# Optimization experiments

Hardware: AMD Instinct MI355X
Metric: run time of the kernel (lower is better)

## Reference

```python
import jax, jax.numpy as jnp
import numpy as np

B, S, E = 4, 2048, 1024
N, H = 16, 64  # n_head, per-head hidden


def setup_inputs() -> dict:
    key = jax.random.key(0)
    k1, k2, k3, k4, k5 = jax.random.split(key, 5)
    scale_in = 1.0 / np.sqrt(E)
    scale_h = 1.0 / np.sqrt(N * H)
    return {
        "x": jax.random.normal(k1, (B, S, E), dtype=jnp.float32),
        "W_qkv": jax.random.uniform(k2, (E, 3 * N * H), minval=-scale_in, maxval=scale_in, dtype=jnp.float32),
        "b_qkv": jax.random.uniform(k3, (3 * N * H,), minval=-scale_in, maxval=scale_in, dtype=jnp.float32),
        "W_out": jax.random.uniform(k4, (N * H, E), minval=-scale_h, maxval=scale_h, dtype=jnp.float32),
        "b_out": jax.random.uniform(k5, (E,), minval=-scale_h, maxval=scale_h, dtype=jnp.float32),
    }


def reference(x, W_qkv, b_qkv, W_out, b_out):
    b, s, e = x.shape
    qkv = x @ W_qkv + b_qkv                      # [B,S,3NH]
    q, k, v = jnp.split(qkv, 3, axis=-1)
    q = q.reshape(b, s, N, H).transpose(0, 2, 1, 3)  # [B,N,S,H]
    k = k.reshape(b, s, N, H).transpose(0, 2, 1, 3)
    v = v.reshape(b, s, N, H).transpose(0, 2, 1, 3)
    inv_scale = jnp.asarray(1.0 / np.sqrt(H), dtype=x.dtype)
    attn = jnp.einsum('bnqh,bnkh->bnqk', q, k) * inv_scale  # [B,N,S,S]
    causal = jnp.tril(jnp.ones((s, s), dtype=bool))
    attn = jnp.where(causal[None, None], attn, jnp.asarray(-jnp.inf, dtype=attn.dtype))
    attn = jax.nn.softmax(attn, axis=-1)
    out = jnp.einsum('bnqk,bnkh->bnqh', attn, v)  # [B,N,S,H]
    out = out.transpose(0, 2, 1, 3).reshape(b, s, N * H)
    return out @ W_out + b_out
```

## Files before the change

kernel.cpp:

```cpp
#include <hip/hip_runtime.h>
#include <hip/hip_bf16.h>

typedef __attribute__((ext_vector_type(8))) short s16x8;
typedef __attribute__((ext_vector_type(4))) short s16x4;
typedef __attribute__((ext_vector_type(4))) float f32x4;

#define MFMA16(a, b, c) __builtin_amdgcn_mfma_f32_16x16x32_bf16(a, b, c, 0, 0, 0)

__device__ __forceinline__ short f2bf(float f) {
  unsigned int x = __builtin_bit_cast(unsigned int, f);
  x += 0x7fffu + ((x >> 16) & 1u);
  return (short)(x >> 16);
}

__device__ __forceinline__ int cperm(int k) {
  return ((k & 12) << 1) | ((k >> 4) << 2) | (k & 3);
}

#define LDT 40

__global__ void cvt_f32_bf16(const float* __restrict__ in, short* __restrict__ out, int n) {
  int idx = blockIdx.x * blockDim.x + threadIdx.x;
  int stride = gridDim.x * blockDim.x;
  for (int i = idx * 4; i < n; i += stride * 4) {
    float4 v = *(const float4*)(in + i);
    s16x4 o;
    o[0] = f2bf(v.x); o[1] = f2bf(v.y); o[2] = f2bf(v.z); o[3] = f2bf(v.w);
    *(s16x4*)(out + i) = o;
  }
}

__global__ __launch_bounds__(256) void gemm_qkv(
    const short* __restrict__ X, const short* __restrict__ W,
    const float* __restrict__ bias,
    short* __restrict__ Qo, short* __restrict__ Ko, short* __restrict__ Vo) {
  const int N = 3072, Kd = 1024;
  __shared__ short As[128 * LDT];
  __shared__ short Bs[128 * LDT];
  int t = threadIdx.x;
  int nTN = N / 128;
  int m0 = (blockIdx.x / nTN) * 128;
  int n0 = (blockIdx.x % nTN) * 128;
  int lane = t & 63, w = t >> 6;
  int wr = (w >> 1) * 64, wc = (w & 1) * 64;
  int r = lane & 15, g = lane >> 4;

  int ar = t >> 1;
  int ak = (t & 1) << 4;
  int bk = t & 31;
  int bc = (t >> 5) << 4;
  int cbk = cperm(bk);

  f32x4 acc[4][4];
  const f32x4 z4 = {0.f, 0.f, 0.f, 0.f};
#pragma unroll
  for (int i = 0; i < 4; ++i)
#pragma unroll
    for (int j = 0; j < 4; ++j) acc[i][j] = z4;

  for (int kt = 0; kt < Kd; kt += 32) {
    if (kt) __syncthreads();
    const short* xr = X + (size_t)(m0 + ar) * Kd + kt + ak;
    s16x8 va0 = *(const s16x8*)(xr);
    s16x8 va1 = *(const s16x8*)(xr + 8);
    short* Ad = &As[ar * LDT];
    *(s16x4*)(Ad + cperm(ak))      = __builtin_shufflevector(va0, va0, 0, 1, 2, 3);
    *(s16x4*)(Ad + cperm(ak + 4))  = __builtin_shufflevector(va0, va0, 4, 5, 6, 7);
    *(s16x4*)(Ad + cperm(ak + 8))  = __builtin_shufflevector(va1, va1, 0, 1, 2, 3);
    *(s16x4*)(Ad + cperm(ak + 12)) = __builtin_shufflevector(va1, va1, 4, 5, 6, 7);
    const short* wrp = W + (size_t)(kt + bk) * N + n0 + bc;
    s16x8 vb0 = *(const s16x8*)(wrp);
    s16x8 vb1 = *(const s16x8*)(wrp + 8);
#pragma unroll
    for (int i = 0; i < 8; ++i) Bs[(bc + i) * LDT + cbk] = vb0[i];
#pragma unroll
    for (int i = 0; i < 8; ++i) Bs[(bc + 8 + i) * LDT + cbk] = vb1[i];
    __syncthreads();

    s16x8 af[4], bfr[4];
#pragma unroll
    for (int mi = 0; mi < 4; ++mi)
      af[mi] = *(const s16x8*)(&As[(wr + mi * 16 + r) * LDT + g * 8]);
#pragma unroll
    for (int ni = 0; ni < 4; ++ni)
      bfr[ni] = *(const s16x8*)(&Bs[(wc + ni * 16 + r) * LDT + g * 8]);
#pragma unroll
    for (int mi = 0; mi < 4; ++mi)
#pragma unroll
      for (int ni = 0; ni < 4; ++ni)
        acc[mi][ni] = MFMA16(af[mi], bfr[ni], acc[mi][ni]);
  }

#pragma unroll
  for (int ni = 0; ni < 4; ++ni) {
    int col = n0 + wc + ni * 16 + r;
    float bv = bias[col];
    int which = col >> 10;
    int rem = col & 1023;
    int head = rem >> 6, h = rem & 63;
    short* dst = (which == 0) ? Qo : (which == 1) ? Ko : Vo;
    float qsc = (which == 0) ? 0.125f * 1.44269504f : 1.0f;
    int hp = (h & 32) | cperm(h & 31);
#pragma unroll
    for (int mi = 0; mi < 4; ++mi)
#pragma unroll
      for (int e = 0; e < 4; ++e) {
        int row = m0 + wr + mi * 16 + g * 4 + e;
        int b = row >> 11, s = row & 2047;
        size_t idx;
        if (which == 2)
          idx = ((size_t)(b * 16 + head) * 64 + h) * 2048 + ((s & ~31) | cperm(s & 31));
        else
          idx = ((size_t)(b * 16 + head) * 2048 + s) * 64 + hp;
        dst[idx] = f2bf((acc[mi][ni][e] + bv) * qsc);
      }
  }
}

__global__ __launch_bounds__(256) void gemm_out(
    const short* __restrict__ X, const short* __restrict__ W,
    const float* __restrict__ bias, float* __restrict__ Out) {
  const int N = 1024, Kd = 1024;
  __shared__ short As[128 * LDT];
  __shared__ short Bs[128 * LDT];
  int t = threadIdx.x;
  int nTN = N / 128;
  int m0 = (blockIdx.x / nTN) * 128;
  int n0 = (blockIdx.x % nTN) * 128;
  int lane = t & 63, w = t >> 6;
  int wr = (w >> 1) * 64, wc = (w & 1) * 64;
  int r = lane & 15, g = lane >> 4;
  int ar = t >> 1, ak = (t & 1) << 4;
  int bk = t & 31, bc = (t >> 5) << 4;
  int cbk = cperm(bk);

  f32x4 acc[4][4];
  const f32x4 z4 = {0.f, 0.f, 0.f, 0.f};
#pragma unroll
  for (int i = 0; i < 4; ++i)
#pragma unroll
    for (int j = 0; j < 4; ++j) acc[i][j] = z4;

  for (int kt = 0; kt < Kd; kt += 32) {
    if (kt) __syncthreads();
    const short* xr = X + (size_t)(m0 + ar) * Kd + kt + ak;
    s16x8 va0 = *(const s16x8*)(xr);
    s16x8 va1 = *(const s16x8*)(xr + 8);
    short* Ad = &As[ar * LDT];
    *(s16x4*)(Ad + cperm(ak))      = __builtin_shufflevector(va0, va0, 0, 1, 2, 3);
    *(s16x4*)(Ad + cperm(ak + 4))  = __builtin_shufflevector(va0, va0, 4, 5, 6, 7);
    *(s16x4*)(Ad + cperm(ak + 8))  = __builtin_shufflevector(va1, va1, 0, 1, 2, 3);
    *(s16x4*)(Ad + cperm(ak + 12)) = __builtin_shufflevector(va1, va1, 4, 5, 6, 7);
    const short* wrp = W + (size_t)(kt + bk) * N + n0 + bc;
    s16x8 vb0 = *(const s16x8*)(wrp);
    s16x8 vb1 = *(const s16x8*)(wrp + 8);
#pragma unroll
    for (int i = 0; i < 8; ++i) Bs[(bc + i) * LDT + cbk] = vb0[i];
#pragma unroll
    for (int i = 0; i < 8; ++i) Bs[(bc + 8 + i) * LDT + cbk] = vb1[i];
    __syncthreads();

    s16x8 af[4], bfr[4];
#pragma unroll
    for (int mi = 0; mi < 4; ++mi)
      af[mi] = *(const s16x8*)(&As[(wr + mi * 16 + r) * LDT + g * 8]);
#pragma unroll
    for (int ni = 0; ni < 4; ++ni)
      bfr[ni] = *(const s16x8*)(&Bs[(wc + ni * 16 + r) * LDT + g * 8]);
#pragma unroll
    for (int mi = 0; mi < 4; ++mi)
#pragma unroll
      for (int ni = 0; ni < 4; ++ni)
        acc[mi][ni] = MFMA16(af[mi], bfr[ni], acc[mi][ni]);
  }

#pragma unroll
  for (int ni = 0; ni < 4; ++ni) {
    int col = n0 + wc + ni * 16 + r;
    float bv = bias[col];
#pragma unroll
    for (int mi = 0; mi < 4; ++mi)
#pragma unroll
      for (int e = 0; e < 4; ++e) {
        int row = m0 + wr + mi * 16 + g * 4 + e;
        Out[(size_t)row * N + col] = acc[mi][ni][e] + bv;
      }
  }
}

__global__ __launch_bounds__(256) void attn(
    const short* __restrict__ Qb, const short* __restrict__ Kb,
    const short* __restrict__ Vt, short* __restrict__ Ob) {
  const int S = 2048, H = 64;
  int bid = blockIdx.x;
  int bn = bid & 63;
  int pr = bid >> 6;
  int batch = bn >> 4, head = bn & 15;
  int t = threadIdx.x, lane = t & 63, w = t >> 6;
  int r = lane & 15, g = lane >> 4;

  const short* Qh = Qb + (size_t)bn * S * H;
  const short* Kh = Kb + (size_t)bn * S * H;
  const short* Vh = Vt + (size_t)bn * S * H;
  const f32x4 z4 = {0.f, 0.f, 0.f, 0.f};

#pragma unroll
  for (int ph = 0; ph < 2; ++ph) {
    int qt = ph ? pr : (15 - pr);
    int q0 = qt * 128;
    int qw = q0 + w * 32;
    int ntiles = qt * 2 + 2;

    s16x8 qf[2][2];
#pragma unroll
    for (int n = 0; n < 2; ++n)
#pragma unroll
      for (int ks = 0; ks < 2; ++ks)
        qf[n][ks] = *(const s16x8*)(Qh + (size_t)(qw + n * 16 + r) * H + ks * 32 + g * 8);

    f32x4 o[2][4];
#pragma unroll
    for (int n = 0; n < 2; ++n)
#pragma unroll
      for (int hb = 0; hb < 4; ++hb) o[n][hb] = z4;
    float mrun[2] = {-__builtin_inff(), -__builtin_inff()};
    float lsum[2] = {0.f, 0.f};

    auto LOADK = [&](int kv0, s16x8 (&kf)[4][2]) {
#pragma unroll
      for (int mp = 0; mp < 4; ++mp)
#pragma unroll
        for (int ks = 0; ks < 2; ++ks)
          kf[mp][ks] = *(const s16x8*)(Kh + (size_t)(kv0 + mp * 16 + r) * H + ks * 32 + g * 8);
    };

    s16x8 kfA[4][2], kfB[4][2];
    LOADK(0, kfA);

    auto TILE = [&](int tt, s16x8 (&kfc)[4][2], s16x8 (&kfn)[4][2]) {
      int kv0 = tt * 64;
      if (kv0 > qw + 31) return;

      s16x8 vf[2][4];
#pragma unroll
      for (int kvh = 0; kvh < 2; ++kvh)
#pragma unroll
        for (int hb = 0; hb < 4; ++hb)
          vf[kvh][hb] = *(const s16x8*)(Vh + (size_t)(hb * 16 + r) * S + kv0 + kvh * 32 + g * 8);

      int tn = tt + 1;
      if (tn < ntiles && tn * 64 <= qw + 31) LOADK(tn * 64, kfn);

      int mpmax = (qw + 31 - kv0) >> 4; if (mpmax > 3) mpmax = 3;
      bool need_mask = (kv0 + 63 > qw);

      float p[4][2][4];
      float rmax[2] = {-__builtin_inff(), -__builtin_inff()};
#pragma unroll
      for (int mp = 0; mp < 4; ++mp) {
        if (mp <= mpmax) {
          f32x4 st[2] = {z4, z4};
#pragma unroll
          for (int n = 0; n < 2; ++n)
#pragma unroll
            for (int ks = 0; ks < 2; ++ks)
              st[n] = MFMA16(kfc[mp][ks], qf[n][ks], st[n]);
#pragma unroll
          for (int n = 0; n < 2; ++n)
#pragma unroll
            for (int e = 0; e < 4; ++e) {
              float v = st[n][e];
              if (need_mask) {
                int kv = kv0 + mp * 16 + g * 4 + e;
                int q = qw + n * 16 + r;
                if (kv > q) v = -__builtin_inff();
              }
              p[mp][n][e] = v;
              rmax[n] = fmaxf(rmax[n], v);
            }
        } else {
#pragma unroll
          for (int n = 0; n < 2; ++n)
#pragma unroll
            for (int e = 0; e < 4; ++e) p[mp][n][e] = 0.f;
        }
      }

#pragma unroll
      for (int n = 0; n < 2; ++n) {
        rmax[n] = fmaxf(rmax[n], __shfl_xor(rmax[n], 16));
        rmax[n] = fmaxf(rmax[n], __shfl_xor(rmax[n], 32));
      }

#pragma unroll
      for (int n = 0; n < 2; ++n) {
        if (!__all(rmax[n] - mrun[n] <= 8.0f)) {
          float mnew = fmaxf(mrun[n], rmax[n]);
          float sc = exp2f(mrun[n] - mnew);
          lsum[n] *= sc;
          mrun[n] = mnew;
#pragma unroll
          for (int e = 0; e < 4; ++e) {
            float bs = __shfl(sc, (lane & 48) + g * 4 + e);
#pragma unroll
            for (int hb = 0; hb < 4; ++hb) o[n][hb][e] *= bs;
          }
        }
      }

#pragma unroll
      for (int mp = 0; mp < 4; ++mp) {
        if (mp <= mpmax) {
#pragma unroll
          for (int n = 0; n < 2; ++n)
#pragma unroll
            for (int e = 0; e < 4; ++e) {
              float ev = exp2f(p[mp][n][e] - mrun[n]);
              p[mp][n][e] = ev;
              lsum[n] += ev;
            }
        }
      }

      int kvhmax = mpmax >> 1;
#pragma unroll
      for (int kvh = 0; kvh < 2; ++kvh) {
        if (kvh > kvhmax) break;
        s16x8 pa[2];
#pragma unroll
        for (int n = 0; n < 2; ++n) {
          s16x8 tmp = {f2bf(p[2 * kvh][n][0]),     f2bf(p[2 * kvh][n][1]),
                       f2bf(p[2 * kvh][n][2]),     f2bf(p[2 * kvh][n][3]),
                       f2bf(p[2 * kvh + 1][n][0]), f2bf(p[2 * kvh + 1][n][1]),
                       f2bf(p[2 * kvh + 1][n][2]), f2bf(p[2 * kvh + 1][n][3])};
          pa[n] = tmp;
        }
#pragma unroll
        for (int hb = 0; hb < 4; ++hb)
#pragma unroll
          for (int n = 0; n < 2; ++n) o[n][hb] = MFMA16(pa[n], vf[kvh][hb], o[n][hb]);
      }
    };

    for (int tt = 0; tt < ntiles; tt += 2) {
      TILE(tt, kfA, kfB);
      TILE(tt + 1, kfB, kfA);
    }

#pragma unroll
    for (int n = 0; n < 2; ++n) {
      float lt = lsum[n];
      lt += __shfl_xor(lt, 16);
      lt += __shfl_xor(lt, 32);
      float il = 1.0f / lt;
#pragma unroll
      for (int e = 0; e < 4; ++e) {
        float bv = __shfl(il, (lane & 48) + g * 4 + e);
        int s = qw + n * 16 + g * 4 + e;
#pragma unroll
        for (int hb = 0; hb < 4; ++hb) {
          int c = head * 64 + hb * 16 + r;
          Ob[(size_t)(batch * 2048 + s) * 1024 + c] = f2bf(o[n][hb][e] * bv);
        }
      }
    }
  }
}

extern "C" void kernel_launch(void* const* d_in, const int* in_sizes, int n_in,
                              void* d_out, int out_size, void* d_ws, size_t ws_size,
                              hipStream_t stream) {
  const float* x    = (const float*)d_in[0];
  const float* Wqkv = (const float*)d_in[1];
  const float* bqkv = (const float*)d_in[2];
  const float* Wout = (const float*)d_in[3];
  const float* bout = (const float*)d_in[4];
  float* out = (float*)d_out;

  char* ws = (char*)d_ws;
  short* Xb    = (short*)(ws);
  short* Wqkvb = (short*)(ws + ((size_t)16 << 20));
  short* Woutb = (short*)(ws + ((size_t)22 << 20));
  short* Qb    = (short*)(ws + ((size_t)24 << 20));
  short* Kb    = (short*)(ws + ((size_t)40 << 20));
  short* Vb    = (short*)(ws + ((size_t)56 << 20));

  cvt_f32_bf16<<<2048, 256, 0, stream>>>(x, Xb, 4 * 2048 * 1024);
  cvt_f32_bf16<<<1024, 256, 0, stream>>>(Wqkv, Wqkvb, 1024 * 3072);
  cvt_f32_bf16<<<512, 256, 0, stream>>>(Wout, Woutb, 1024 * 1024);

  gemm_qkv<<<64 * 24, 256, 0, stream>>>(Xb, Wqkvb, bqkv, Qb, Kb, Vb);
  attn<<<512, 256, 0, stream>>>(Qb, Kb, Vb, Xb);
  gemm_out<<<64 * 8, 256, 0, stream>>>(Xb, Woutb, bout, out);
}
```

Measured before the change: 299.0 us.

## Split attention work per wave across paired query tiles and double the grid

After: 382.1 us. 27.8% more time.

```diff
diff --git a/kernel.cpp b/kernel.cpp
--- a/kernel.cpp
+++ b/kernel.cpp
@@ -188,180 +188,161 @@
   }
 }
 
-__global__ __launch_bounds__(256) void attn(
+__global__ __launch_bounds__(256, 4) void attn(
     const short* __restrict__ Qb, const short* __restrict__ Kb,
     const short* __restrict__ Vt, short* __restrict__ Ob) {
   const int S = 2048, H = 64;
   int bid = blockIdx.x;
+  int j = bid >> 6;
   int bn = bid & 63;
-  int pr = bid >> 6;
   int batch = bn >> 4, head = bn & 15;
   int t = threadIdx.x, lane = t & 63, w = t >> 6;
   int r = lane & 15, g = lane >> 4;
+  int qt = (w < 2) ? j : (15 - j);
+  int qw = qt * 128 + w * 32;
+  int ntw = ((qw + 31) >> 6) + 1;
 
   const short* Qh = Qb + (size_t)bn * S * H;
   const short* Kh = Kb + (size_t)bn * S * H;
   const short* Vh = Vt + (size_t)bn * S * H;
   const f32x4 z4 = {0.f, 0.f, 0.f, 0.f};
 
-#pragma unroll
-  for (int ph = 0; ph < 2; ++ph) {
-    int qt = ph ? pr : (15 - pr);
-    int q0 = qt * 128;
-    int qw = q0 + w * 32;
-    int ntiles = qt * 2 + 2;
-
-    s16x8 qf[2][2];
-#pragma unroll
-    for (int n = 0; n < 2; ++n)
+  s16x8 qf[2][2];
+#pragma unroll
+  for (int n = 0; n < 2; ++n)
+#pragma unroll
+    for (int ks = 0; ks < 2; ++ks)
+      qf[n][ks] = *(const s16x8*)(Qh + (size_t)(qw + n * 16 + r) * H + ks * 32 + g * 8);
+
+  f32x4 o[2][4];
+#pragma unroll
+  for (int n = 0; n < 2; ++n)
+#pragma unroll
+    for (int hb = 0; hb < 4; ++hb) o[n][hb] = z4;
+  float mrun[2] = {-__builtin_inff(), -__builtin_inff()};
+  float lsum[2] = {0.f, 0.f};
+
+  for (int tt = 0; tt < ntw; ++tt) {
+    int kv0 = tt * 64;
+    bool need_mask = (kv0 + 63 > qw);
+    int mpmax = (qw + 31 - kv0) >> 4; if (mpmax > 3) mpmax = 3;
+
+    s16x8 kf[4][2];
+#pragma unroll
+    for (int mp = 0; mp < 4; ++mp)
 #pragma unroll
       for (int ks = 0; ks < 2; ++ks)
-        qf[n][ks] = *(const s16x8*)(Qh + (size_t)(qw + n * 16 + r) * H + ks * 32 + g * 8);
-
-    f32x4 o[2][4];
-#pragma unroll
-    for (int n = 0; n < 2; ++n)
-#pragma unroll
-      for (int hb = 0; hb < 4; ++hb) o[n][hb] = z4;
-    float mrun[2] = {-__builtin_inff(), -__builtin_inff()};
-    float lsum[2] = {0.f, 0.f};
-
-    auto LOADK = [&](int kv0, s16x8 (&kf)[4][2]) {
-#pragma unroll
-      for (int mp = 0; mp < 4; ++mp)
-#pragma unroll
-        for (int ks = 0; ks < 2; ++ks)
-          kf[mp][ks] = *(const s16x8*)(Kh + (size_t)(kv0 + mp * 16 + r) * H + ks * 32 + g * 8);
-    };
-
-    s16x8 kfA[4][2], kfB[4][2];
-    LOADK(0, kfA);
-
-    auto TILE = [&](int tt, s16x8 (&kfc)[4][2], s16x8 (&kfn)[4][2]) {
-      int kv0 = tt * 64;
-      if (kv0 > qw + 31) return;
-
-      s16x8 vf[2][4];
-#pragma unroll
-      for (int kvh = 0; kvh < 2; ++kvh)
-#pragma unroll
-        for (int hb = 0; hb < 4; ++hb)
-          vf[kvh][hb] = *(const s16x8*)(Vh + (size_t)(hb * 16 + r) * S + kv0 + kvh * 32 + g * 8);
-
-      int tn = tt + 1;
-      if (tn < ntiles && tn * 64 <= qw + 31) LOADK(tn * 64, kfn);
-
-      int mpmax = (qw + 31 - kv0) >> 4; if (mpmax > 3) mpmax = 3;
-      bool need_mask = (kv0 + 63 > qw);
-
-      float p[4][2][4];
-      float rmax[2] = {-__builtin_inff(), -__builtin_inff()};
-#pragma unroll
-      for (int mp = 0; mp < 4; ++mp) {
-        if (mp <= mpmax) {
-          f32x4 st[2] = {z4, z4};
-#pragma unroll
-          for (int n = 0; n < 2; ++n)
-#pragma unroll
-            for (int ks = 0; ks < 2; ++ks)
-              st[n] = MFMA16(kfc[mp][ks], qf[n][ks], st[n]);
-#pragma unroll
-          for (int n = 0; n < 2; ++n)
-#pragma unroll
-            for (int e = 0; e < 4; ++e) {
-              float v = st[n][e];
-              if (need_mask) {
-                int kv = kv0 + mp * 16 + g * 4 + e;
-                int q = qw + n * 16 + r;
-                if (kv > q) v = -__builtin_inff();
-              }
-              p[mp][n][e] = v;
-              rmax[n] = fmaxf(rmax[n], v);
+        kf[mp][ks] = *(const s16x8*)(Kh + (size_t)(kv0 + mp * 16 + r) * H + ks * 32 + g * 8);
+
+    s16x8 vf[2][4];
+#pragma unroll
+    for (int kvh = 0; kvh < 2; ++kvh)
+#pragma unroll
+      for (int hb = 0; hb < 4; ++hb)
+        vf[kvh][hb] = *(const s16x8*)(Vh + (size_t)(hb * 16 + r) * S + kv0 + kvh * 32 + g * 8);
+
+    float p[4][2][4];
+    float rmax[2] = {-__builtin_inff(), -__builtin_inff()};
+#pragma unroll
+    for (int mp = 0; mp < 4; ++mp) {
+      if (mp <= mpmax) {
+        f32x4 st[2] = {z4, z4};
+#pragma unroll
+        for (int n = 0; n < 2; ++n)
+#pragma unroll
+          for (int ks = 0; ks < 2; ++ks)
+            st[n] = MFMA16(kf[mp][ks], qf[n][ks], st[n]);
+#pragma unroll
+        for (int n = 0; n < 2; ++n)
+#pragma unroll
+          for (int e = 0; e < 4; ++e) {
+            float v = st[n][e];
+            if (need_mask) {
+              int kv = kv0 + mp * 16 + g * 4 + e;
+              int q = qw + n * 16 + r;
+              if (kv > q) v = -__builtin_inff();
             }
-        } else {
-#pragma unroll
-          for (int n = 0; n < 2; ++n)
-#pragma unroll
-            for (int e = 0; e < 4; ++e) p[mp][n][e] = 0.f;
+            p[mp][n][e] = v;
+            rmax[n] = fmaxf(rmax[n], v);
+          }
+      } else {
+#pragma unroll
+        for (int n = 0; n < 2; ++n)
+#pragma unroll
+          for (int e = 0; e < 4; ++e) p[mp][n][e] = 0.f;
+      }
+    }
+
+#pragma unroll
+    for (int n = 0; n < 2; ++n) {
+      rmax[n] = fmaxf(rmax[n], __shfl_xor(rmax[n], 16));
+      rmax[n] = fmaxf(rmax[n], __shfl_xor(rmax[n], 32));
+    }
+
+#pragma unroll
+    for (int n = 0; n < 2; ++n) {
+      if (!__all(rmax[n] - mrun[n] <= 8.0f)) {
+        float mnew = fmaxf(mrun[n], rmax[n]);
+        float sc = exp2f(mrun[n] - mnew);
+        lsum[n] *= sc;
+        mrun[n] = mnew;
+#pragma unroll
+        for (int e = 0; e < 4; ++e) {
+          float bs = __shfl(sc, (lane & 48) + g * 4 + e);
+#pragma unroll
+          for (int hb = 0; hb < 4; ++hb) o[n][hb][e] *= bs;
         }
       }
-
+    }
+
+#pragma unroll
+    for (int mp = 0; mp < 4; ++mp) {
+      if (mp <= mpmax) {
+#pragma unroll
+        for (int n = 0; n < 2; ++n)
+#pragma unroll
+          for (int e = 0; e < 4; ++e) {
+            float ev = exp2f(p[mp][n][e] - mrun[n]);
+            p[mp][n][e] = ev;
+            lsum[n] += ev;
+          }
+      }
+    }
+
+    int kvhmax = mpmax >> 1;
+#pragma unroll
+    for (int kvh = 0; kvh < 2; ++kvh) {
+      if (kvh > kvhmax) break;
+      s16x8 pa[2];
 #pragma unroll
       for (int n = 0; n < 2; ++n) {
-        rmax[n] = fmaxf(rmax[n], __shfl_xor(rmax[n], 16));
-        rmax[n] = fmaxf(rmax[n], __shfl_xor(rmax[n], 32));
-      }
-
-#pragma unroll
-      for (int n = 0; n < 2; ++n) {
-        if (!__all(rmax[n] - mrun[n] <= 8.0f)) {
-          float mnew = fmaxf(mrun[n], rmax[n]);
-          float sc = exp2f(mrun[n] - mnew);
-          lsum[n] *= sc;
-          mrun[n] = mnew;
-#pragma unroll
-          for (int e = 0; e < 4; ++e) {
-            float bs = __shfl(sc, (lane & 48) + g * 4 + e);
-#pragma unroll
-            for (int hb = 0; hb < 4; ++hb) o[n][hb][e] *= bs;
-          }
-        }
-      }
-
-#pragma unroll
-      for (int mp = 0; mp < 4; ++mp) {
-        if (mp <= mpmax) {
-#pragma unroll
-          for (int n = 0; n < 2; ++n)
-#pragma unroll
-            for (int e = 0; e < 4; ++e) {
-              float ev = exp2f(p[mp][n][e] - mrun[n]);
-              p[mp][n][e] = ev;
-              lsum[n] += ev;
-            }
-        }
-      }
-
-      int kvhmax = mpmax >> 1;
-#pragma unroll
-      for (int kvh = 0; kvh < 2; ++kvh) {
-        if (kvh > kvhmax) break;
-        s16x8 pa[2];
-#pragma unroll
-        for (int n = 0; n < 2; ++n) {
-          s16x8 tmp = {f2bf(p[2 * kvh][n][0]),     f2bf(p[2 * kvh][n][1]),
-                       f2bf(p[2 * kvh][n][2]),     f2bf(p[2 * kvh][n][3]),
-                       f2bf(p[2 * kvh + 1][n][0]), f2bf(p[2 * kvh + 1][n][1]),
-                       f2bf(p[2 * kvh + 1][n][2]), f2bf(p[2 * kvh + 1][n][3])};
-          pa[n] = tmp;
-        }
-#pragma unroll
-        for (int hb = 0; hb < 4; ++hb)
-#pragma unroll
-          for (int n = 0; n < 2; ++n) o[n][hb] = MFMA16(pa[n], vf[kvh][hb], o[n][hb]);
-      }
-    };
-
-    for (int tt = 0; tt < ntiles; tt += 2) {
-      TILE(tt, kfA, kfB);
-      TILE(tt + 1, kfB, kfA);
-    }
-
-#pragma unroll
-    for (int n = 0; n < 2; ++n) {
-      float lt = lsum[n];
-      lt += __shfl_xor(lt, 16);
-      lt += __shfl_xor(lt, 32);
-      float il = 1.0f / lt;
-#pragma unroll
-      for (int e = 0; e < 4; ++e) {
-        float bv = __shfl(il, (lane & 48) + g * 4 + e);
-        int s = qw + n * 16 + g * 4 + e;
-#pragma unroll
-        for (int hb = 0; hb < 4; ++hb) {
-          int c = head * 64 + hb * 16 + r;
-          Ob[(size_t)(batch * 2048 + s) * 1024 + c] = f2bf(o[n][hb][e] * bv);
-        }
+        s16x8 tmp = {f2bf(p[2 * kvh][n][0]),     f2bf(p[2 * kvh][n][1]),
+                     f2bf(p[2 * kvh][n][2]),     f2bf(p[2 * kvh][n][3]),
+                     f2bf(p[2 * kvh + 1][n][0]), f2bf(p[2 * kvh + 1][n][1]),
+                     f2bf(p[2 * kvh + 1][n][2]), f2bf(p[2 * kvh + 1][n][3])};
+        pa[n] = tmp;
+      }
+#pragma unroll
+      for (int hb = 0; hb < 4; ++hb)
+#pragma unroll
+        for (int n = 0; n < 2; ++n) o[n][hb] = MFMA16(pa[n], vf[kvh][hb], o[n][hb]);
+    }
+  }
+
+#pragma unroll
+  for (int n = 0; n < 2; ++n) {
+    float lt = lsum[n];
+    lt += __shfl_xor(lt, 16);
+    lt += __shfl_xor(lt, 32);
+    float il = 1.0f / lt;
+#pragma unroll
+    for (int e = 0; e < 4; ++e) {
+      float bv = __shfl(il, (lane & 48) + g * 4 + e);
+      int s = qw + n * 16 + g * 4 + e;
+#pragma unroll
+      for (int hb = 0; hb < 4; ++hb) {
+        int c = head * 64 + hb * 16 + r;
+        Ob[(size_t)(batch * 2048 + s) * 1024 + c] = f2bf(o[n][hb][e] * bv);
       }
     }
   }
@@ -390,6 +371,6 @@
   cvt_f32_bf16<<<512, 256, 0, stream>>>(Wout, Woutb, 1024 * 1024);
 
   gemm_qkv<<<64 * 24, 256, 0, stream>>>(Xb, Wqkvb, bqkv, Qb, Kb, Vb);
-  attn<<<512, 256, 0, stream>>>(Qb, Kb, Vb, Xb);
+  attn<<<1024, 256, 0, stream>>>(Qb, Kb, Vb, Xb);
   gemm_out<<<64 * 8, 256, 0, stream>>>(Xb, Woutb, bout, out);
 }
```
